# Performance work log

Hardware: AMD Instinct MI355X
Metric: run time of the kernel (lower is better)

## Reference

```python
import jax, jax.numpy as jnp
import numpy as np

N, E, D, H = 50000, 800000, 128, 8
EPS = 1e-8       # softmax denominator eps from propagate_attention
LN_EPS = 1e-5    # torch LayerNorm default
NEG_SLOPE = 0.01 # torch leaky_relu default


def setup_inputs() -> dict:
    key = jax.random.key(0)
    ks = jax.random.split(key, 16)
    s = 0.02
    inp = {
        'x': jax.random.normal(ks[0], (N, D), jnp.float32),
        'y': jax.random.normal(ks[1], (E, D), jnp.float32),
        'src': jax.random.randint(ks[2], (E,), 0, N, jnp.int32),
        'dst': jax.random.randint(ks[3], (E,), 0, N, jnp.int32),
        'Wq': jax.random.normal(ks[4], (D, D), jnp.float32) * s,
        'bq': jnp.zeros((D,), jnp.float32),
        'Wk': jax.random.normal(ks[5], (D, D), jnp.float32) * s,
        'bk': jnp.zeros((D,), jnp.float32),
        'Wv': jax.random.normal(ks[6], (D, D), jnp.float32) * s,
        'bv': jnp.zeros((D,), jnp.float32),
        'We': jax.random.normal(ks[7], (D, D), jnp.float32) * s,
        'be': jnp.zeros((D,), jnp.float32),
        'Wr': jax.random.normal(ks[8], (D, D), jnp.float32) * s,
        'br': jnp.zeros((D,), jnp.float32),
        'Wg': jax.random.normal(ks[9], (3 * D, D), jnp.float32) * s,
        'bg': jnp.zeros((D,), jnp.float32),
        'ln_g': jnp.ones((D,), jnp.float32),
        'ln_b': jnp.zeros((D,), jnp.float32),
    }
    return inp


def reference(x, y, src, dst, Wq, bq, Wk, bk, Wv, bv, We, be, Wr, br, Wg, bg, ln_g, ln_b):
    n, dm = x.shape
    ne = y.shape[0]
    h = H
    d = dm // h
    # node/edge projections, multi-head split
    q = (x @ Wq + bq).reshape(n, h, d)
    k = (x @ Wk + bk).reshape(n, h, d)
    v = (x @ Wv + bv).reshape(n, h, d)
    e = (y @ We + be).reshape(ne, h, d)
    # u_add_e then v_dot_e: score[e,h] = q[dst] . (k[src] + e)
    ke = k[src] + e                                   # [E,h,d]
    score = jnp.einsum('ehd,ehd->eh', q[dst], ke)[..., None]  # [E,h,1]
    escore = jnp.exp(score)
    # segment softmax denominator z per destination node
    z = jax.ops.segment_sum(escore, dst, num_segments=n)       # [N,h,1]
    norm_escore = (1.0 / jnp.sqrt(jnp.float32(d))) * escore / (EPS + z[dst])  # dropout is identity (eval)
    # weighted message (v[src] + e) scatter-summed to dst
    ve = v[src] + e                                   # [E,h,d]
    o = jax.ops.segment_sum(norm_escore * ve, dst, num_segments=n).reshape(n, dm)
    # gated residual update (aggregate='concat')
    r = x @ Wr + br
    cat = jnp.concatenate([o, r, o - r], axis=1)      # [N,3D]
    b = jax.nn.sigmoid(cat @ Wg + bg)
    hmix = o - b * o + b * r
    mu = hmix.mean(-1, keepdims=True)
    var = hmix.var(-1, keepdims=True)
    ln = (hmix - mu) * jax.lax.rsqrt(var + LN_EPS) * ln_g + ln_b
    x_out = jnp.where(ln >= 0, ln, NEG_SLOPE * ln)    # leaky_relu
    return x_out, norm_escore
```

## Files before the change

kernel.cpp:

```cpp
#include <hip/hip_runtime.h>

#define DEV __device__ __forceinline__

typedef __bf16 bf16_t;
typedef bf16_t bf16x8 __attribute__((ext_vector_type(8)));
typedef bf16_t bf16x4 __attribute__((ext_vector_type(4)));
typedef float  f32x4  __attribute__((ext_vector_type(4)));

constexpr int D  = 128;
constexpr int H  = 8;
constexpr int HD = 16;
constexpr float EPS_Z   = 1e-8f;
constexpr float LN_EPS  = 1e-5f;
constexpr float NEG     = 0.01f;
constexpr float INV_SQD = 0.25f;

__global__ void k_zero_ints(int* p, long n) {
  long i = (long)blockIdx.x * blockDim.x + threadIdx.x;
  long st = (long)gridDim.x * blockDim.x;
  for (; i < n; i += st) p[i] = 0;
}

__global__ void k_count(const int* __restrict__ dst, int* __restrict__ cnt, int E_) {
  int i = blockIdx.x * blockDim.x + threadIdx.x;
  if (i < E_) atomicAdd(&cnt[dst[i]], 1);
}

__global__ void k_scan_part(const int* __restrict__ cnt, int* __restrict__ bsum, int N_) {
  __shared__ int s[256];
  int i = blockIdx.x * 256 + threadIdx.x;
  s[threadIdx.x] = (i < N_) ? cnt[i] : 0;
  __syncthreads();
  for (int off = 128; off > 0; off >>= 1) {
    if (threadIdx.x < off) s[threadIdx.x] += s[threadIdx.x + off];
    __syncthreads();
  }
  if (threadIdx.x == 0) bsum[blockIdx.x] = s[0];
}

__global__ void k_scan_mid(int* bsum, int nb) {
  if (threadIdx.x == 0 && blockIdx.x == 0) {
    int run = 0;
    for (int i = 0; i < nb; ++i) { int v = bsum[i]; bsum[i] = run; run += v; }
  }
}

__global__ void k_scan_fin(const int* __restrict__ cnt, const int* __restrict__ bsum,
                           int* __restrict__ offs, int N_, int E_) {
  __shared__ int s[256];
  int i = blockIdx.x * 256 + threadIdx.x;
  int v = (i < N_) ? cnt[i] : 0;
  s[threadIdx.x] = v;
  __syncthreads();
  for (int off = 1; off < 256; off <<= 1) {
    int y = (threadIdx.x >= off) ? s[threadIdx.x - off] : 0;
    __syncthreads();
    s[threadIdx.x] += y;
    __syncthreads();
  }
  if (i < N_) offs[i] = bsum[blockIdx.x] + s[threadIdx.x] - v;
  if (blockIdx.x == 0 && threadIdx.x == 0) offs[N_] = E_;
}

__global__ void k_scatter(const int* __restrict__ dst, const int* __restrict__ offs,
                          int* __restrict__ cursor, int* __restrict__ eids, int E_) {
  int i = blockIdx.x * blockDim.x + threadIdx.x;
  if (i < E_) {
    int dn = dst[i];
    int pos = offs[dn] + atomicAdd(&cursor[dn], 1);
    eids[pos] = i;
  }
}

struct PackArgs {
  const float* W[6];
  bf16_t* hi[6];
  bf16_t* lo[6];
  int K[6];
};

__global__ __launch_bounds__(256)
void k_packw(PackArgs pa) {
  int wid = blockIdx.y;
  int K = pa.K[wid];
  int tid = blockIdx.x * 256 + threadIdx.x;
  if (tid >= K * 16) return;
  int lane = tid & 63;
  int tt = tid >> 6;
  int ct = tt & 7, kc = tt >> 3;
  int col = ct * 16 + (lane & 15);
  int kbase = kc * 32 + (lane >> 4) * 8;
  const float* W = pa.W[wid];
  bf16_t* ph = pa.hi[wid] + (size_t)tid * 8;
  bf16_t* pl = pa.lo[wid] + (size_t)tid * 8;
#pragma unroll
  for (int j = 0; j < 8; ++j) {
    float f = W[(size_t)(kbase + j) * D + col];
    bf16_t h = (bf16_t)f;
    bf16_t l = (bf16_t)(f - (float)h);
    ph[j] = h;
    pl[j] = l;
  }
}

DEV int swzA(int row, int kbyte) { return (row * 256 + kbyte) ^ ((row & 7) << 4); }

DEV void stage_split_row(float f0, float f1, float f2, float f3,
                         char* hb, char* lb, int off) {
  bf16x4 h, l;
  h[0] = (bf16_t)f0; l[0] = (bf16_t)(f0 - (float)h[0]);
  h[1] = (bf16_t)f1; l[1] = (bf16_t)(f1 - (float)h[1]);
  h[2] = (bf16_t)f2; l[2] = (bf16_t)(f2 - (float)h[2]);
  h[3] = (bf16_t)f3; l[3] = (bf16_t)(f3 - (float)h[3]);
  *(bf16x4*)(hb + off) = h;
  *(bf16x4*)(lb + off) = l;
}

template<int EPI>
DEV void mfma_gemm_body(const float* __restrict__ A,
                        const bf16_t* __restrict__ pkh, const bf16_t* __restrict__ pkl,
                        const float* __restrict__ bias,
                        float* __restrict__ Cf, bf16_t* __restrict__ Cb, int M,
                        const int* __restrict__ src, const int* __restrict__ dst,
                        const float* __restrict__ qm, const float* __restrict__ km,
                        float* __restrict__ escore, char* smem) {
  char* ahi = smem;
  char* alo = smem + 16384;
  float* e_s = (float*)smem;
  const int t = threadIdx.x;
  const int row0 = blockIdx.x * 64;

#pragma unroll
  for (int i = 0; i < 8; ++i) {
    int f = t + i * 256;
    int row = f >> 5, c4 = f & 31;
    float4 v4 = make_float4(0.f, 0.f, 0.f, 0.f);
    if (row0 + row < M) v4 = *(const float4*)(A + (size_t)(row0 + row) * D + c4 * 4);
    stage_split_row(v4.x, v4.y, v4.z, v4.w, ahi, alo, swzA(row, c4 * 8));
  }
  __syncthreads();

  const int lane = t & 63, w = t >> 6;
  const int fr = lane & 15, fg = lane >> 4;
  f32x4 acc[8];
#pragma unroll
  for (int ct = 0; ct < 8; ++ct) acc[ct] = (f32x4){0.f, 0.f, 0.f, 0.f};

  const bf16x8* Ph = (const bf16x8*)pkh + lane;
  const bf16x8* Pl = (const bf16x8*)pkl + lane;
#pragma unroll
  for (int kc = 0; kc < 4; ++kc) {
    int aoff = swzA(w * 16 + fr, kc * 64 + fg * 16);
    bf16x8 ah = *(const bf16x8*)(ahi + aoff);
    bf16x8 al = *(const bf16x8*)(alo + aoff);
    const bf16x8* ph = Ph + kc * 512;
    const bf16x8* pl = Pl + kc * 512;
#pragma unroll
    for (int ct = 0; ct < 8; ++ct) {
      bf16x8 wh = ph[ct * 64];
      bf16x8 wl = pl[ct * 64];
      acc[ct] = __builtin_amdgcn_mfma_f32_16x16x32_bf16(ah, wh, acc[ct], 0, 0, 0);
      acc[ct] = __builtin_amdgcn_mfma_f32_16x16x32_bf16(al, wh, acc[ct], 0, 0, 0);
      acc[ct] = __builtin_amdgcn_mfma_f32_16x16x32_bf16(ah, wl, acc[ct], 0, 0, 0);
    }
  }
  __syncthreads();

#pragma unroll
  for (int ct = 0; ct < 8; ++ct) {
    int col = ct * 16 + fr;
    float b = bias[col];
#pragma unroll
    for (int p = 0; p < 4; ++p) {
      int row = w * 16 + fg * 4 + p;
      e_s[row * 132 + col] = acc[ct][p] + b;
    }
  }
  __syncthreads();

  if (EPI == 0) {
#pragma unroll
    for (int i = 0; i < 8; ++i) {
      int f = t + i * 256;
      int row = f >> 5, c4 = f & 31;
      if (row0 + row < M)
        *(float4*)(Cf + (size_t)(row0 + row) * D + c4 * 4) =
            *(const float4*)&e_s[row * 132 + c4 * 4];
    }
  } else {
#pragma unroll
    for (int i = 0; i < 8; ++i) {
      int f = t + i * 256;
      int row = f >> 5, c4 = f & 31;
      if (row0 + row < M) {
        float4 ev = *(const float4*)&e_s[row * 132 + c4 * 4];
        bf16x4 h;
        h[0] = (bf16_t)ev.x; h[1] = (bf16_t)ev.y;
        h[2] = (bf16_t)ev.z; h[3] = (bf16_t)ev.w;
        *(bf16x4*)(Cb + (size_t)(row0 + row) * D + c4 * 4) = h;
      }
    }
#pragma unroll
    for (int pp = 0; pp < 2; ++pp) {
      int p = t + pp * 256;
      int row = p >> 3, h = p & 7;
      int grow = row0 + row;
      if (grow < M) {
        int s_ = src[grow], d_ = dst[grow];
        const float* qp = qm + (size_t)d_ * D + h * HD;
        const float* kp = km + (size_t)s_ * D + h * HD;
        float sc = 0.f;
#pragma unroll
        for (int i2 = 0; i2 < 4; ++i2) {
          float4 qv = *(const float4*)(qp + i2 * 4);
          float4 kv = *(const float4*)(kp + i2 * 4);
          float4 ev = *(const float4*)&e_s[row * 132 + h * HD + i2 * 4];
          sc += qv.x * (kv.x + ev.x) + qv.y * (kv.y + ev.y) +
                qv.z * (kv.z + ev.z) + qv.w * (kv.w + ev.w);
        }
        escore[(size_t)grow * H + h] = expf(sc);
      }
    }
  }
}

struct NP {
  const bf16_t* pkh[4];
  const bf16_t* pkl[4];
  const float*  b[4];
  float*        C[4];
};

__global__ __launch_bounds__(256)
void k_nodeproj(const float* __restrict__ x, NP np, int M) {
  __shared__ __align__(16) char smem[64 * 132 * 4];
  int wi = blockIdx.y;
  mfma_gemm_body<0>(x, np.pkh[wi], np.pkl[wi], np.b[wi], np.C[wi], nullptr, M,
                    nullptr, nullptr, nullptr, nullptr, nullptr, smem);
}

__global__ __launch_bounds__(256)
void k_gemm_edge(const float* __restrict__ y,
                 const bf16_t* __restrict__ pkh, const bf16_t* __restrict__ pkl,
                 const float* __restrict__ be, bf16_t* __restrict__ e, int M,
                 const int* __restrict__ src, const int* __restrict__ dst,
                 const float* __restrict__ q, const float* __restrict__ k,
                 float* __restrict__ esc) {
  __shared__ __align__(16) char smem[64 * 132 * 4];
  mfma_gemm_body<1>(y, pkh, pkl, be, nullptr, e, M, src, dst, q, k, esc, smem);
}

__global__ __launch_bounds__(128)
void k_gather(const int* __restrict__ eids_all, const int* __restrict__ offs,
              const int* __restrict__ src, const float* __restrict__ vmat,
              const bf16_t* __restrict__ emat, const float* __restrict__ escore,
              float* __restrict__ o, float* __restrict__ out_ns) {
  int nid = blockIdx.x;
  int t = threadIdx.x;
  int h = t >> 4;
  int beg = offs[nid], end = offs[nid + 1];
  __shared__ int eids[128];
  __shared__ int srcs[128];
  float z0 = 0.f, z1 = 0.f;
  for (int c0 = beg; c0 < end; c0 += 128) {
    int cnt = min(128, end - c0);
    __syncthreads();
    if (t < cnt) eids[t] = eids_all[c0 + t];
    __syncthreads();
    int j = 0;
    for (; j + 1 < cnt; j += 2) {
      z0 += escore[(size_t)eids[j] * H + h];
      z1 += escore[(size_t)eids[j + 1] * H + h];
    }
    if (j < cnt) z0 += escore[(size_t)eids[j] * H + h];
  }
  float inv = INV_SQD / (EPS_Z + (z0 + z1));
  float acc0 = 0.f, acc1 = 0.f;
  for (int c0 = beg; c0 < end; c0 += 128) {
    int cnt = min(128, end - c0);
    __syncthreads();
    if (t < cnt) { int e_ = eids_all[c0 + t]; eids[t] = e_; srcs[t] = src[e_]; }
    __syncthreads();
    int j = 0;
    for (; j + 1 < cnt; j += 2) {
      int e0 = eids[j], e1 = eids[j + 1];
      float es0 = escore[(size_t)e0 * H + h];
      float es1 = escore[(size_t)e1 * H + h];
      float ev0 = (float)emat[(size_t)e0 * D + t];
      float ev1 = (float)emat[(size_t)e1 * D + t];
      float vv0 = vmat[(size_t)srcs[j] * D + t];
      float vv1 = vmat[(size_t)srcs[j + 1] * D + t];
      float ns0 = es0 * inv, ns1 = es1 * inv;
      if ((t & 15) == 0) {
        out_ns[(size_t)e0 * H + h] = ns0;
        out_ns[(size_t)e1 * H + h] = ns1;
      }
      acc0 += ns0 * (vv0 + ev0);
      acc1 += ns1 * (vv1 + ev1);
    }
    if (j < cnt) {
      int e0 = eids[j];
      float es0 = escore[(size_t)e0 * H + h];
      float ev0 = (float)emat[(size_t)e0 * D + t];
      float vv0 = vmat[(size_t)srcs[j] * D + t];
      float ns0 = es0 * inv;
      if ((t & 15) == 0) out_ns[(size_t)e0 * H + h] = ns0;
      acc0 += ns0 * (vv0 + ev0);
    }
  }
  o[(size_t)nid * D + t] = acc0 + acc1;
}

__global__ __launch_bounds__(256)
void k_final(const float* __restrict__ o, const float* __restrict__ r,
             const bf16_t* __restrict__ pkg,
             const float* __restrict__ bg,
             const float* __restrict__ lng, const float* __restrict__ lnb,
             float* __restrict__ xout, int M) {
  __shared__ __align__(16) char smem[3 * 64 * 128 * 2];
  float* e_s = (float*)smem;
  const int t = threadIdx.x;
  const int row0 = blockIdx.x * 64;

#pragma unroll
  for (int i = 0; i < 8; ++i) {
    int f = t + i * 256;
    int row = f >> 5, c4 = f & 31;
    float4 ov = make_float4(0.f, 0.f, 0.f, 0.f), rv = ov;
    if (row0 + row < M) {
      ov = *(const float4*)(o + (size_t)(row0 + row) * D + c4 * 4);
      rv = *(const float4*)(r + (size_t)(row0 + row) * D + c4 * 4);
    }
    int off = swzA(row, c4 * 8);
    bf16x4 hv;
    hv[0] = (bf16_t)ov.x; hv[1] = (bf16_t)ov.y; hv[2] = (bf16_t)ov.z; hv[3] = (bf16_t)ov.w;
    *(bf16x4*)(smem + off) = hv;
    hv[0] = (bf16_t)rv.x; hv[1] = (bf16_t)rv.y; hv[2] = (bf16_t)rv.z; hv[3] = (bf16_t)rv.w;
    *(bf16x4*)(smem + 16384 + off) = hv;
    hv[0] = (bf16_t)(ov.x - rv.x); hv[1] = (bf16_t)(ov.y - rv.y);
    hv[2] = (bf16_t)(ov.z - rv.z); hv[3] = (bf16_t)(ov.w - rv.w);
    *(bf16x4*)(smem + 32768 + off) = hv;
  }
  __syncthreads();

  const int lane = t & 63, w = t >> 6;
  const int fr = lane & 15, fg = lane >> 4;
  f32x4 acc[8];
#pragma unroll
  for (int ct = 0; ct < 8; ++ct) acc[ct] = (f32x4){0.f, 0.f, 0.f, 0.f};

#pragma unroll
  for (int s = 0; s < 3; ++s) {
    char* base = smem + s * 16384;
    const bf16x8* Ph = (const bf16x8*)pkg + lane + s * 2048;
#pragma unroll
    for (int kc = 0; kc < 4; ++kc) {
      bf16x8 ah = *(const bf16x8*)(base + swzA(w * 16 + fr, kc * 64 + fg * 16));
      const bf16x8* ph = Ph + kc * 512;
#pragma unroll
      for (int ct = 0; ct < 8; ++ct)
        acc[ct] = __builtin_amdgcn_mfma_f32_16x16x32_bf16(ah, ph[ct * 64], acc[ct], 0, 0, 0);
    }
  }
  __syncthreads();

#pragma unroll
  for (int ct = 0; ct < 8; ++ct) {
    int col = ct * 16 + fr;
    float b = bg[col];
#pragma unroll
    for (int p = 0; p < 4; ++p) {
      int row = w * 16 + fg * 4 + p;
      e_s[row * 132 + col] = acc[ct][p] + b;
    }
  }
  __syncthreads();

#pragma unroll
  for (int i = 0; i < 8; ++i) {
    int f = t + i * 256;
    int row = f >> 5, c4 = f & 31;
    int grow = row0 + row;
    float4 g4 = *(const float4*)&e_s[row * 132 + c4 * 4];
    float4 ov = make_float4(0.f, 0.f, 0.f, 0.f), rv = ov;
    if (grow < M) {
      ov = *(const float4*)(o + (size_t)grow * D + c4 * 4);
      rv = *(const float4*)(r + (size_t)grow * D + c4 * 4);
    }
    float b0 = 1.f / (1.f + expf(-g4.x));
    float b1 = 1.f / (1.f + expf(-g4.y));
    float b2 = 1.f / (1.f + expf(-g4.z));
    float b3 = 1.f / (1.f + expf(-g4.w));
    float h0 = ov.x + b0 * (rv.x - ov.x);
    float h1 = ov.y + b1 * (rv.y - ov.y);
    float h2 = ov.z + b2 * (rv.z - ov.z);
    float h3 = ov.w + b3 * (rv.w - ov.w);
    float s1 = h0 + h1 + h2 + h3;
#pragma unroll
    for (int m = 1; m < 32; m <<= 1) s1 += __shfl_xor(s1, m);
    float mu = s1 * (1.f / 128.f);
    float d0 = h0 - mu, d1 = h1 - mu, d2 = h2 - mu, d3 = h3 - mu;
    float s2 = d0 * d0 + d1 * d1 + d2 * d2 + d3 * d3;
#pragma unroll
    for (int m = 1; m < 32; m <<= 1) s2 += __shfl_xor(s2, m);
    float rsig = rsqrtf(s2 * (1.f / 128.f) + LN_EPS);
    float4 gv  = *(const float4*)(lng + c4 * 4);
    float4 bv2 = *(const float4*)(lnb + c4 * 4);
    float4 res;
    res.x = d0 * rsig * gv.x + bv2.x;
    res.y = d1 * rsig * gv.y + bv2.y;
    res.z = d2 * rsig * gv.z + bv2.z;
    res.w = d3 * rsig * gv.w + bv2.w;
    res.x = res.x >= 0.f ? res.x : NEG * res.x;
    res.y = res.y >= 0.f ? res.y : NEG * res.y;
    res.z = res.z >= 0.f ? res.z : NEG * res.z;
    res.w = res.w >= 0.f ? res.w : NEG * res.w;
    if (grow < M)
      *(float4*)(xout + (size_t)grow * D + c4 * 4) = res;
  }
}

extern "C" void kernel_launch(void* const* d_in, const int* in_sizes, int n_in,
                              void* d_out, int out_size, void* d_ws, size_t ws_size,
                              hipStream_t stream) {
  const float* x   = (const float*)d_in[0];
  const float* y   = (const float*)d_in[1];
  const int*   src = (const int*)d_in[2];
  const int*   dst = (const int*)d_in[3];
  const float* Wq = (const float*)d_in[4];  const float* bq = (const float*)d_in[5];
  const float* Wk = (const float*)d_in[6];  const float* bk = (const float*)d_in[7];
  const float* Wv = (const float*)d_in[8];  const float* bv = (const float*)d_in[9];
  const float* We = (const float*)d_in[10]; const float* be = (const float*)d_in[11];
  const float* Wr = (const float*)d_in[12]; const float* br = (const float*)d_in[13];
  const float* Wg = (const float*)d_in[14]; const float* bg = (const float*)d_in[15];
  const float* lng = (const float*)d_in[16]; const float* lnb = (const float*)d_in[17];

  const int N = in_sizes[0] / D;
  const int E = in_sizes[2];

  float* xout   = (float*)d_out;
  float* out_ns = (float*)d_out + (size_t)N * D;

  char* w = (char*)d_ws;
  auto alloc = [&](size_t bytes) -> char* {
    char* p = w;
    w += (bytes + 255) & ~(size_t)255;
    return p;
  };
  float* q  = (float*)alloc((size_t)N * D * 4);
  float* k  = (float*)alloc((size_t)N * D * 4);
  float* v  = (float*)alloc((size_t)N * D * 4);
  float* r  = (float*)alloc((size_t)N * D * 4);
  float* o  = (float*)alloc((size_t)N * D * 4);
  float* escore = (float*)alloc((size_t)E * H * 4);
  int* cnt    = (int*)alloc((size_t)N * 4);
  int* offs   = (int*)alloc((size_t)(N + 1) * 4);
  int* cursor = (int*)alloc((size_t)N * 4);
  int* eids   = (int*)alloc((size_t)E * 4);
  int* bsum   = (int*)alloc(4096);
  bf16_t* pk_hi[6];
  bf16_t* pk_lo[6];
  const float* Ws[6] = {Wq, Wk, Wv, Wr, We, Wg};
  int Ks[6] = {D, D, D, D, D, 3 * D};
  for (int i = 0; i < 6; ++i) {
    pk_hi[i] = (bf16_t*)alloc((size_t)Ks[i] * D * 2);
    pk_lo[i] = (bf16_t*)alloc((size_t)Ks[i] * D * 2);
  }
  bf16_t* e = (bf16_t*)alloc((size_t)E * D * 2);
  if ((size_t)(w - (char*)d_ws) > ws_size) return;

  PackArgs pa;
  for (int i = 0; i < 6; ++i) {
    pa.W[i] = Ws[i]; pa.hi[i] = pk_hi[i]; pa.lo[i] = pk_lo[i]; pa.K[i] = Ks[i];
  }
  k_packw<<<dim3(24, 6), 256, 0, stream>>>(pa);

  int nb_scan = (N + 255) / 256;
  k_zero_ints<<<256, 256, 0, stream>>>(cnt, N);
  k_zero_ints<<<256, 256, 0, stream>>>(cursor, N);
  k_count<<<(E + 255) / 256, 256, 0, stream>>>(dst, cnt, E);
  k_scan_part<<<nb_scan, 256, 0, stream>>>(cnt, bsum, N);
  k_scan_mid<<<1, 1, 0, stream>>>(bsum, nb_scan);
  k_scan_fin<<<nb_scan, 256, 0, stream>>>(cnt, bsum, offs, N, E);
  k_scatter<<<(E + 255) / 256, 256, 0, stream>>>(dst, offs, cursor, eids, E);

  int nbn = (N + 63) / 64;
  NP np;
  np.pkh[0] = pk_hi[0]; np.pkl[0] = pk_lo[0]; np.b[0] = bq; np.C[0] = q;
  np.pkh[1] = pk_hi[1]; np.pkl[1] = pk_lo[1]; np.b[1] = bk; np.C[1] = k;
  np.pkh[2] = pk_hi[2]; np.pkl[2] = pk_lo[2]; np.b[2] = bv; np.C[2] = v;
  np.pkh[3] = pk_hi[3]; np.pkl[3] = pk_lo[3]; np.b[3] = br; np.C[3] = r;
  k_nodeproj<<<dim3(nbn, 4), 256, 0, stream>>>(x, np, N);

  int nbe = (E + 63) / 64;
  k_gemm_edge<<<nbe, 256, 0, stream>>>(y, pk_hi[4], pk_lo[4], be, e, E,
                                       src, dst, q, k, escore);

  k_gather<<<N, 128, 0, stream>>>(eids, offs, src, v, e, escore, o, out_ns);

  k_final<<<nbn, 256, 0, stream>>>(o, r, pk_hi[5], bg, lng, lnb, xout, N);
}
```

Measured before the change: 1.206 ms.

## Split edge GEMM, score, gather and normalisation into persistent and streaming kernels

The edge projection becomes a persistent-grid GEMM that prefetches the next tile's input into registers while computing the current one, and it writes bf16 output through a bf16 LDS staging buffer. Score computation moves to its own per-(edge, head) kernel that reads e back from memory. The gather now does one pass that accumulates both the softmax denominator and the unnormalised message, instead of two passes over the edges. It writes per-node inverse denominators, and a new streaming kernel produces the normalised scores. This trades an extra read of e and escore and two more launches for fewer gather passes and a more overlapped edge GEMM.

```diff
diff --git a/kernel.cpp b/kernel.cpp
--- a/kernel.cpp
+++ b/kernel.cpp
@@ -9,7 +9,6 @@
 
 constexpr int D  = 128;
 constexpr int H  = 8;
-constexpr int HD = 16;
 constexpr float EPS_Z   = 1e-8f;
 constexpr float LN_EPS  = 1e-5f;
 constexpr float NEG     = 0.01f;
@@ -116,17 +115,24 @@
   *(bf16x4*)(lb + off) = l;
 }
 
-template<int EPI>
-DEV void mfma_gemm_body(const float* __restrict__ A,
-                        const bf16_t* __restrict__ pkh, const bf16_t* __restrict__ pkl,
-                        const float* __restrict__ bias,
-                        float* __restrict__ Cf, bf16_t* __restrict__ Cb, int M,
-                        const int* __restrict__ src, const int* __restrict__ dst,
-                        const float* __restrict__ qm, const float* __restrict__ km,
-                        float* __restrict__ escore, char* smem) {
+struct NP {
+  const bf16_t* pkh[4];
+  const bf16_t* pkl[4];
+  const float*  b[4];
+  float*        C[4];
+};
+
+__global__ __launch_bounds__(256)
+void k_nodeproj(const float* __restrict__ A, NP np, int M) {
+  __shared__ __align__(16) char smem[64 * 132 * 4];
   char* ahi = smem;
   char* alo = smem + 16384;
   float* e_s = (float*)smem;
+  const int wi = blockIdx.y;
+  const bf16_t* pkh = np.pkh[wi];
+  const bf16_t* pkl = np.pkl[wi];
+  const float* bias = np.b[wi];
+  float* Cf = np.C[wi];
   const int t = threadIdx.x;
   const int row0 = blockIdx.x * 64;
 
@@ -177,138 +183,202 @@
     }
   }
   __syncthreads();
-
-  if (EPI == 0) {
+#pragma unroll
+  for (int i = 0; i < 8; ++i) {
+    int f = t + i * 256;
+    int row = f >> 5, c4 = f & 31;
+    if (row0 + row < M)
+      *(float4*)(Cf + (size_t)(row0 + row) * D + c4 * 4) =
+          *(const float4*)&e_s[row * 132 + c4 * 4];
+  }
+}
+
+__global__ __launch_bounds__(256)
+void k_gemm_edge(const float* __restrict__ A,
+                 const bf16_t* __restrict__ pkh, const bf16_t* __restrict__ pkl,
+                 const float* __restrict__ bias, bf16_t* __restrict__ C,
+                 int M, int ntiles) {
+  __shared__ __align__(16) char smem[32768];
+  char* ahi = smem;
+  char* alo = smem + 16384;
+  bf16_t* e_s = (bf16_t*)smem;
+  const int t = threadIdx.x;
+  const int lane = t & 63, w = t >> 6;
+  const int fr = lane & 15, fg = lane >> 4;
+
+  float bfrag[8];
+#pragma unroll
+  for (int ct = 0; ct < 8; ++ct) bfrag[ct] = bias[ct * 16 + fr];
+
+  const bf16x8* Ph = (const bf16x8*)pkh + lane;
+  const bf16x8* Pl = (const bf16x8*)pkl + lane;
+
+  float4 sreg[8];
+  int tile = blockIdx.x;
+  if (tile < ntiles) {
+    int row0 = tile * 64;
 #pragma unroll
     for (int i = 0; i < 8; ++i) {
-      int f = t + i * 256;
-      int row = f >> 5, c4 = f & 31;
+      int f = t + i * 256, row = f >> 5, c4 = f & 31;
+      sreg[i] = (row0 + row < M) ? *(const float4*)(A + (size_t)(row0 + row) * D + c4 * 4)
+                                 : make_float4(0.f, 0.f, 0.f, 0.f);
+    }
+  }
+  while (tile < ntiles) {
+    int row0 = tile * 64;
+    __syncthreads();
+#pragma unroll
+    for (int i = 0; i < 8; ++i) {
+      int f = t + i * 256, row = f >> 5, c4 = f & 31;
+      stage_split_row(sreg[i].x, sreg[i].y, sreg[i].z, sreg[i].w, ahi, alo,
+                      swzA(row, c4 * 8));
+    }
+    __syncthreads();
+    bf16x8 ah[4], al[4];
+#pragma unroll
+    for (int kc = 0; kc < 4; ++kc) {
+      int aoff = swzA(w * 16 + fr, kc * 64 + fg * 16);
+      ah[kc] = *(const bf16x8*)(ahi + aoff);
+      al[kc] = *(const bf16x8*)(alo + aoff);
+    }
+    int ntile = tile + gridDim.x;
+    if (ntile < ntiles) {
+      int nrow0 = ntile * 64;
+#pragma unroll
+      for (int i = 0; i < 8; ++i) {
+        int f = t + i * 256, row = f >> 5, c4 = f & 31;
+        sreg[i] = (nrow0 + row < M)
+                      ? *(const float4*)(A + (size_t)(nrow0 + row) * D + c4 * 4)
+                      : make_float4(0.f, 0.f, 0.f, 0.f);
+      }
+    }
+    f32x4 acc[8];
+#pragma unroll
+    for (int ct = 0; ct < 8; ++ct) acc[ct] = (f32x4){0.f, 0.f, 0.f, 0.f};
+#pragma unroll
+    for (int kc = 0; kc < 4; ++kc) {
+      const bf16x8* ph = Ph + kc * 512;
+      const bf16x8* pl = Pl + kc * 512;
+#pragma unroll
+      for (int ct = 0; ct < 8; ++ct) {
+        bf16x8 wh = ph[ct * 64];
+        bf16x8 wl = pl[ct * 64];
+        acc[ct] = __builtin_amdgcn_mfma_f32_16x16x32_bf16(ah[kc], wh, acc[ct], 0, 0, 0);
+        acc[ct] = __builtin_amdgcn_mfma_f32_16x16x32_bf16(al[kc], wh, acc[ct], 0, 0, 0);
+        acc[ct] = __builtin_amdgcn_mfma_f32_16x16x32_bf16(ah[kc], wl, acc[ct], 0, 0, 0);
+      }
+    }
+    __syncthreads();
+#pragma unroll
+    for (int ct = 0; ct < 8; ++ct) {
+      int col = ct * 16 + fr;
+#pragma unroll
+      for (int p = 0; p < 4; ++p) {
+        int row = w * 16 + fg * 4 + p;
+        e_s[row * 136 + col] = (bf16_t)(acc[ct][p] + bfrag[ct]);
+      }
+    }
+    __syncthreads();
+#pragma unroll
+    for (int i = 0; i < 4; ++i) {
+      int row = i * 16 + (t >> 4), c8 = t & 15;
       if (row0 + row < M)
-        *(float4*)(Cf + (size_t)(row0 + row) * D + c4 * 4) =
-            *(const float4*)&e_s[row * 132 + c4 * 4];
-    }
-  } else {
-#pragma unroll
-    for (int i = 0; i < 8; ++i) {
-      int f = t + i * 256;
-      int row = f >> 5, c4 = f & 31;
-      if (row0 + row < M) {
-        float4 ev = *(const float4*)&e_s[row * 132 + c4 * 4];
-        bf16x4 h;
-        h[0] = (bf16_t)ev.x; h[1] = (bf16_t)ev.y;
-        h[2] = (bf16_t)ev.z; h[3] = (bf16_t)ev.w;
-        *(bf16x4*)(Cb + (size_t)(row0 + row) * D + c4 * 4) = h;
-      }
-    }
-#pragma unroll
-    for (int pp = 0; pp < 2; ++pp) {
-      int p = t + pp * 256;
-      int row = p >> 3, h = p & 7;
-      int grow = row0 + row;
-      if (grow < M) {
-        int s_ = src[grow], d_ = dst[grow];
-        const float* qp = qm + (size_t)d_ * D + h * HD;
-        const float* kp = km + (size_t)s_ * D + h * HD;
-        float sc = 0.f;
-#pragma unroll
-        for (int i2 = 0; i2 < 4; ++i2) {
-          float4 qv = *(const float4*)(qp + i2 * 4);
-          float4 kv = *(const float4*)(kp + i2 * 4);
-          float4 ev = *(const float4*)&e_s[row * 132 + h * HD + i2 * 4];
-          sc += qv.x * (kv.x + ev.x) + qv.y * (kv.y + ev.y) +
-                qv.z * (kv.z + ev.z) + qv.w * (kv.w + ev.w);
-        }
-        escore[(size_t)grow * H + h] = expf(sc);
-      }
-    }
-  }
-}
-
-struct NP {
-  const bf16_t* pkh[4];
-  const bf16_t* pkl[4];
-  const float*  b[4];
-  float*        C[4];
-};
+        *(bf16x8*)(C + (size_t)(row0 + row) * D + c8 * 8) =
+            *(const bf16x8*)&e_s[row * 136 + c8 * 8];
+    }
+    tile = ntile;
+  }
+}
 
 __global__ __launch_bounds__(256)
-void k_nodeproj(const float* __restrict__ x, NP np, int M) {
-  __shared__ __align__(16) char smem[64 * 132 * 4];
-  int wi = blockIdx.y;
-  mfma_gemm_body<0>(x, np.pkh[wi], np.pkl[wi], np.b[wi], np.C[wi], nullptr, M,
-                    nullptr, nullptr, nullptr, nullptr, nullptr, smem);
-}
-
-__global__ __launch_bounds__(256)
-void k_gemm_edge(const float* __restrict__ y,
-                 const bf16_t* __restrict__ pkh, const bf16_t* __restrict__ pkl,
-                 const float* __restrict__ be, bf16_t* __restrict__ e, int M,
-                 const int* __restrict__ src, const int* __restrict__ dst,
-                 const float* __restrict__ q, const float* __restrict__ k,
-                 float* __restrict__ esc) {
-  __shared__ __align__(16) char smem[64 * 132 * 4];
-  mfma_gemm_body<1>(y, pkh, pkl, be, nullptr, e, M, src, dst, q, k, esc, smem);
+void k_score(const int* __restrict__ src, const int* __restrict__ dst,
+             const float* __restrict__ q, const float* __restrict__ k,
+             const bf16_t* __restrict__ e, float* __restrict__ escore, int E_) {
+  int tid = blockIdx.x * 256 + threadIdx.x;
+  if (tid >= E_ * H) return;
+  int eg = tid >> 3, h = tid & 7;
+  int s_ = src[eg], d_ = dst[eg];
+  const float* qp = q + (size_t)d_ * D + h * 16;
+  const float* kp = k + (size_t)s_ * D + h * 16;
+  const bf16_t* ep = e + (size_t)eg * D + h * 16;
+  bf16x8 e0 = *(const bf16x8*)ep;
+  bf16x8 e1 = *(const bf16x8*)(ep + 8);
+  float sc = 0.f;
+#pragma unroll
+  for (int i = 0; i < 2; ++i) {
+    float4 qv = *(const float4*)(qp + i * 4);
+    float4 kv = *(const float4*)(kp + i * 4);
+    sc += qv.x * (kv.x + (float)e0[i * 4 + 0]) + qv.y * (kv.y + (float)e0[i * 4 + 1]) +
+          qv.z * (kv.z + (float)e0[i * 4 + 2]) + qv.w * (kv.w + (float)e0[i * 4 + 3]);
+  }
+#pragma unroll
+  for (int i = 0; i < 2; ++i) {
+    float4 qv = *(const float4*)(qp + 8 + i * 4);
+    float4 kv = *(const float4*)(kp + 8 + i * 4);
+    sc += qv.x * (kv.x + (float)e1[i * 4 + 0]) + qv.y * (kv.y + (float)e1[i * 4 + 1]) +
+          qv.z * (kv.z + (float)e1[i * 4 + 2]) + qv.w * (kv.w + (float)e1[i * 4 + 3]);
+  }
+  escore[tid] = expf(sc);
 }
 
 __global__ __launch_bounds__(128)
 void k_gather(const int* __restrict__ eids_all, const int* __restrict__ offs,
               const int* __restrict__ src, const float* __restrict__ vmat,
               const bf16_t* __restrict__ emat, const float* __restrict__ escore,
-              float* __restrict__ o, float* __restrict__ out_ns) {
+              float* __restrict__ o, float* __restrict__ invz) {
   int nid = blockIdx.x;
   int t = threadIdx.x;
   int h = t >> 4;
   int beg = offs[nid], end = offs[nid + 1];
   __shared__ int eids[128];
   __shared__ int srcs[128];
-  float z0 = 0.f, z1 = 0.f;
+  float z = 0.f, acc = 0.f;
   for (int c0 = beg; c0 < end; c0 += 128) {
     int cnt = min(128, end - c0);
     __syncthreads();
-    if (t < cnt) eids[t] = eids_all[c0 + t];
+    if (t < cnt) { int e_ = eids_all[c0 + t]; eids[t] = e_; srcs[t] = src[e_]; }
     __syncthreads();
     int j = 0;
-    for (; j + 1 < cnt; j += 2) {
-      z0 += escore[(size_t)eids[j] * H + h];
-      z1 += escore[(size_t)eids[j + 1] * H + h];
-    }
-    if (j < cnt) z0 += escore[(size_t)eids[j] * H + h];
-  }
-  float inv = INV_SQD / (EPS_Z + (z0 + z1));
-  float acc0 = 0.f, acc1 = 0.f;
-  for (int c0 = beg; c0 < end; c0 += 128) {
-    int cnt = min(128, end - c0);
-    __syncthreads();
-    if (t < cnt) { int e_ = eids_all[c0 + t]; eids[t] = e_; srcs[t] = src[e_]; }
-    __syncthreads();
-    int j = 0;
-    for (; j + 1 < cnt; j += 2) {
-      int e0 = eids[j], e1 = eids[j + 1];
+    for (; j + 3 < cnt; j += 4) {
+      int e0 = eids[j], e1 = eids[j + 1], e2 = eids[j + 2], e3 = eids[j + 3];
       float es0 = escore[(size_t)e0 * H + h];
       float es1 = escore[(size_t)e1 * H + h];
+      float es2 = escore[(size_t)e2 * H + h];
+      float es3 = escore[(size_t)e3 * H + h];
       float ev0 = (float)emat[(size_t)e0 * D + t];
       float ev1 = (float)emat[(size_t)e1 * D + t];
+      float ev2 = (float)emat[(size_t)e2 * D + t];
+      float ev3 = (float)emat[(size_t)e3 * D + t];
       float vv0 = vmat[(size_t)srcs[j] * D + t];
       float vv1 = vmat[(size_t)srcs[j + 1] * D + t];
-      float ns0 = es0 * inv, ns1 = es1 * inv;
-      if ((t & 15) == 0) {
-        out_ns[(size_t)e0 * H + h] = ns0;
-        out_ns[(size_t)e1 * H + h] = ns1;
-      }
-      acc0 += ns0 * (vv0 + ev0);
-      acc1 += ns1 * (vv1 + ev1);
-    }
-    if (j < cnt) {
+      float vv2 = vmat[(size_t)srcs[j + 2] * D + t];
+      float vv3 = vmat[(size_t)srcs[j + 3] * D + t];
+      z += (es0 + es1) + (es2 + es3);
+      acc += es0 * (vv0 + ev0) + es1 * (vv1 + ev1) +
+             es2 * (vv2 + ev2) + es3 * (vv3 + ev3);
+    }
+    for (; j < cnt; ++j) {
       int e0 = eids[j];
       float es0 = escore[(size_t)e0 * H + h];
       float ev0 = (float)emat[(size_t)e0 * D + t];
       float vv0 = vmat[(size_t)srcs[j] * D + t];
-      float ns0 = es0 * inv;
-      if ((t & 15) == 0) out_ns[(size_t)e0 * H + h] = ns0;
-      acc0 += ns0 * (vv0 + ev0);
-    }
-  }
-  o[(size_t)nid * D + t] = acc0 + acc1;
+      z += es0;
+      acc += es0 * (vv0 + ev0);
+    }
+  }
+  float inv = INV_SQD / (EPS_Z + z);
+  o[(size_t)nid * D + t] = acc * inv;
+  if ((t & 15) == 0) invz[(size_t)nid * H + h] = inv;
+}
+
+__global__ __launch_bounds__(256)
+void k_ns(const int* __restrict__ dst, const float* __restrict__ escore,
+          const float* __restrict__ invz, float* __restrict__ out_ns, int EH) {
+  int i = blockIdx.x * 256 + threadIdx.x;
+  if (i < EH) {
+    int eg = i >> 3, h = i & 7;
+    out_ns[i] = escore[i] * invz[(size_t)dst[eg] * H + h];
+  }
 }
 
 __global__ __launch_bounds__(256)
@@ -453,6 +523,7 @@
   float* r  = (float*)alloc((size_t)N * D * 4);
   float* o  = (float*)alloc((size_t)N * D * 4);
   float* escore = (float*)alloc((size_t)E * H * 4);
+  float* invz   = (float*)alloc((size_t)N * H * 4);
   int* cnt    = (int*)alloc((size_t)N * 4);
   int* offs   = (int*)alloc((size_t)(N + 1) * 4);
   int* cursor = (int*)alloc((size_t)N * 4);
@@ -492,11 +563,15 @@
   np.pkh[3] = pk_hi[3]; np.pkl[3] = pk_lo[3]; np.b[3] = br; np.C[3] = r;
   k_nodeproj<<<dim3(nbn, 4), 256, 0, stream>>>(x, np, N);
 
-  int nbe = (E + 63) / 64;
-  k_gemm_edge<<<nbe, 256, 0, stream>>>(y, pk_hi[4], pk_lo[4], be, e, E,
-                                       src, dst, q, k, escore);
-
-  k_gather<<<N, 128, 0, stream>>>(eids, offs, src, v, e, escore, o, out_ns);
+  int ntiles = (E + 63) / 64;
+  int nbe = ntiles < 2500 ? ntiles : 2500;
+  k_gemm_edge<<<nbe, 256, 0, stream>>>(y, pk_hi[4], pk_lo[4], be, e, E, ntiles);
+
+  k_score<<<(E * H + 255) / 256, 256, 0, stream>>>(src, dst, q, k, e, escore, E);
+
+  k_gather<<<N, 128, 0, stream>>>(eids, offs, src, v, e, escore, o, invz);
+
+  k_ns<<<(E * H + 255) / 256, 256, 0, stream>>>(dst, escore, invz, out_ns, E * H);
 
   k_final<<<nbn, 256, 0, stream>>>(o, r, pk_hi[5], bg, lng, lnb, xout, N);
 }
```

New measurement: 1.092 ms. -9.5%, faster.
